# Kernel optimization log

Hardware: AMD Instinct MI355X
Metric: run time of the kernel (lower is better)

The kernel has to match this reference:

```python
import jax, jax.numpy as jnp
import numpy as np

B, L, H, D_IN = 64, 4096, 128, 3

def setup_inputs() -> dict:
    key = jax.random.key(0)
    ks = jax.random.split(key, 9)
    def lin_w(k, fan_in, shape):
        bound = 1.0 / np.sqrt(fan_in)
        return jax.random.uniform(k, shape, jnp.float32, -bound, bound)
    return {
        "x": jax.random.normal(ks[0], (B, L, D_IN), jnp.float32),
        "Wp": lin_w(ks[1], D_IN, (D_IN, H)), "bp": lin_w(ks[2], D_IN, (H,)),
        "Wz": lin_w(ks[3], H, (H, H)),      "bz": lin_w(ks[4], H, (H,)),
        "Wh": lin_w(ks[5], H, (H, H)),      "bh": lin_w(ks[6], H, (H,)),
        "Wg": lin_w(ks[7], H, (H, 1)),      "bg": lin_w(ks[8], H, (1,)),
    }

def reference(x, Wp, bp, Wz, bz, Wh, bh, Wg, bg):
    # Batched projections across all timesteps (B, L, H)
    inp = x @ Wp + bp                      # input_proj
    z = jax.nn.sigmoid(inp @ Wz + bz)      # update gate
    h_tilde = jnp.tanh(inp @ Wh + bh)      # candidate
    # Linear recurrence h_t = a_t * h_{t-1} + b_t, h_{-1} = 0
    a = 1.0 - z
    b = z * h_tilde
    def combine(c1, c2):
        a1, b1 = c1
        a2, b2 = c2
        return (a1 * a2, b1 * a2 + b2)
    _, h = jax.lax.associative_scan(combine, (a, b), axis=1)  # h_t (since h_{-1}=0)
    # Readout uses h BEFORE the update at each step: preds_t = gauss_head(h_{t-1})
    h_prev = jnp.concatenate([jnp.zeros_like(h[:, :1]), h[:, :-1]], axis=1)
    preds = h_prev @ Wg + bg               # (B, L, 1)
    return preds
```

## Files before the change

### kernel.cpp

```cpp
#include <hip/hip_runtime.h>
#include <hip/hip_bf16.h>
#include <stdint.h>

#define B_   64
#define L_   4096
#define H_   128
#define T_   64
#define C_   (L_/T_)
#define BH_  (B_*H_)
#define PADI 136

typedef __attribute__((ext_vector_type(8))) short short8;
typedef __attribute__((ext_vector_type(4))) short short4v;
typedef __attribute__((ext_vector_type(4))) float floatx4;
typedef __attribute__((ext_vector_type(2))) float floatx2;

#define LOG2E 1.44269504088896340736f

__device__ __forceinline__ unsigned short f2bf(float f){
    unsigned int u = __float_as_uint(f);
    u += 0x7FFFu + ((u >> 16) & 1u);
    return (unsigned short)(u >> 16);
}
__device__ __forceinline__ float bf2f(unsigned short s){
    return __uint_as_float(((unsigned int)s) << 16);
}

__global__ void prep_w(const float* __restrict__ Wz, const float* __restrict__ Wh,
                       unsigned short* __restrict__ WzT, unsigned short* __restrict__ WhT){
    int b = blockIdx.x;
    const float* W = (b < 16) ? Wz : Wh;
    unsigned short* WT = (b < 16) ? WzT : WhT;
    int b16 = b & 15, tid = threadIdx.x;
    #pragma unroll
    for (int it = 0; it < 4; ++it){
        int idx = b16*1024 + it*256 + tid;
        int n = idx >> 7, k = idx & 127;
        WT[idx] = f2bf(W[k*H_ + n]);
    }
}

__global__ __launch_bounds__(256, 4)
void carry_kogge(const floatx2* __restrict__ agg2, float* __restrict__ carry_g){
    const int row  = blockIdx.x*4 + (threadIdx.x >> 6);
    const int lane = threadIdx.x & 63;
    floatx2 v = agg2[(size_t)row*C_ + lane];
    #pragma unroll
    for (int d = 1; d < 64; d <<= 1){
        float oA = __shfl_up(v[0], d, 64);
        float oH = __shfl_up(v[1], d, 64);
        if (lane >= d){
            v[1] = fmaf(oH, v[0], v[1]);
            v[0] = oA * v[0];
        }
    }
    float eh = __shfl_up(v[1], 1, 64);
    carry_g[(size_t)row*C_ + lane] = (lane == 0) ? 0.0f : eh;
}


__global__ __launch_bounds__(256, 4)
void gates_agg(const float* __restrict__ x,
               const float* __restrict__ Wp, const float* __restrict__ bp,
               const float* __restrict__ bz, const float* __restrict__ bh,
               const float* __restrict__ Wg,
               const unsigned short* __restrict__ WzT,
               const unsigned short* __restrict__ WhT,
               floatx2* __restrict__ agg2,
               float* __restrict__ sloc, unsigned short* __restrict__ pw_g)
{
    __shared__ __align__(16) unsigned short s_ab[H_*H_];
    __shared__ float s_bz[H_], s_bh[H_], s_wg[H_];
    __shared__ float s_part[256];
    unsigned short* inp_lds = s_ab;

    const int bid = blockIdx.x;
    const int bb  = bid / C_;
    const int cc  = bid % C_;
    const int t0g = cc * T_;
    const int tid = threadIdx.x;
    const int wv = tid >> 6, lane = tid & 63, quad = lane >> 4, l15 = lane & 15;

    if (tid < H_){ s_bz[tid] = bz[tid]; s_bh[tid] = bh[tid]; s_wg[tid] = Wg[tid]; }

    {
        const int h0 = (tid & 15) * 8;
        float w0[8], w1[8], w2[8], b0[8];
        #pragma unroll
        for (int m = 0; m < 8; ++m){
            w0[m] = Wp[h0+m]; w1[m] = Wp[H_+h0+m]; w2[m] = Wp[2*H_+h0+m];
            b0[m] = bp[h0+m];
        }
        #pragma unroll
        for (int it = 0; it < 4; ++it){
            int t = (tid >> 4) + it*16;
            const float* xr = x + ((size_t)bb*L_ + t0g + t)*3;
            float x0 = xr[0], x1 = xr[1], x2 = xr[2];
            short8 pk;
            #pragma unroll
            for (int m = 0; m < 8; ++m){
                float v = b0[m];
                v = fmaf(x0, w0[m], v);
                v = fmaf(x1, w1[m], v);
                v = fmaf(x2, w2[m], v);
                pk[m] = (short)f2bf(v);
            }
            *(short8*)&inp_lds[t*PADI + h0] = pk;
        }
    }
    __syncthreads();

    const int ct0 = wv*2;

    floatx4 accz[4][2], acch[4][2];
    #pragma unroll
    for (int r = 0; r < 4; ++r)
        #pragma unroll
        for (int c = 0; c < 2; ++c){
            accz[r][c] = (floatx4){0.f,0.f,0.f,0.f};
            acch[r][c] = (floatx4){0.f,0.f,0.f,0.f};
        }
    #pragma unroll
    for (int kk = 0; kk < 4; ++kk){
        short8 af[4], bz_[2], bh_[2];
        #pragma unroll
        for (int r = 0; r < 4; ++r)
            af[r] = *(const short8*)&inp_lds[(r*16 + l15)*PADI + kk*32 + quad*8];
        #pragma unroll
        for (int c = 0; c < 2; ++c){
            bz_[c] = *(const short8*)&WzT[((ct0+c)*16 + l15)*H_ + kk*32 + quad*8];
            bh_[c] = *(const short8*)&WhT[((ct0+c)*16 + l15)*H_ + kk*32 + quad*8];
        }
        #pragma unroll
        for (int r = 0; r < 4; ++r)
            #pragma unroll
            for (int c = 0; c < 2; ++c){
                accz[r][c] = __builtin_amdgcn_mfma_f32_16x16x32_bf16(af[r], bz_[c], accz[r][c], 0, 0, 0);
                acch[r][c] = __builtin_amdgcn_mfma_f32_16x16x32_bf16(af[r], bh_[c], acch[r][c], 0, 0, 0);
            }
    }
    __syncthreads();

    #pragma unroll
    for (int r = 0; r < 4; ++r){
        #pragma unroll
        for (int c = 0; c < 2; ++c){
            int col = (ct0+c)*16 + l15;
            float vbz = s_bz[col], vbh = s_bh[col];
            short8 pk;
            #pragma unroll
            for (int e = 0; e < 4; ++e){
                float szb = accz[r][c][e] + vbz;
                float a = __builtin_amdgcn_rcpf(1.0f + __builtin_amdgcn_exp2f(szb * LOG2E));
                float shb = acch[r][c][e] + vbh;
                float ex = __builtin_amdgcn_exp2f(2.0f*LOG2E*shb);
                float th = 1.0f - 2.0f*__builtin_amdgcn_rcpf(ex + 1.0f);
                float bt = (1.0f - a) * th;
                pk[2*e]   = (short)f2bf(a);
                pk[2*e+1] = (short)f2bf(bt);
            }
            int ch = (r*4 + quad) ^ l15;
            *(short8*)&s_ab[col*H_ + ch*8] = pk;
        }
    }
    __syncthreads();

    if (tid < H_){
        float A = 1.0f, h = 0.0f;
        float wgv = s_wg[tid];
        #pragma unroll
        for (int t4 = 0; t4 < 16; ++t4){
            int base = tid*H_ + ((t4 ^ (tid & 15)) << 3);
            short8 pr = *(const short8*)&s_ab[base];
            short8 wb;
            #pragma unroll
            for (int e = 0; e < 4; ++e){
                float aa = bf2f((unsigned short)pr[2*e]);
                float bv = bf2f((unsigned short)pr[2*e+1]);
                wb[2*e]   = (short)f2bf(h * wgv);
                wb[2*e+1] = (short)f2bf(A * wgv);
                A *= aa;
                h = fmaf(aa, h, bv);
            }
            *(short8*)&s_ab[base] = wb;
        }
        agg2[(size_t)(bb*H_ + tid)*C_ + cc] = (floatx2){A, h};
    }
    __syncthreads();

    {
        unsigned short* dst = pw_g + (size_t)bid*(T_*H_);
        #pragma unroll
        for (int i = 0; i < 8; ++i){
            int idx = i*256 + tid;
            int col = idx >> 4, t4 = idx & 15;
            short8 pr = *(const short8*)&s_ab[col*H_ + ((t4 ^ (col & 15)) << 3)];
            short4v pw4;
            pw4[0] = pr[1]; pw4[1] = pr[3]; pw4[2] = pr[5]; pw4[3] = pr[7];
            *(short4v*)&dst[col*T_ + t4*4] = pw4;
        }
    }

    {
        int t = tid & 63, w4 = tid >> 6;
        int t4 = t >> 2, e2 = (t & 3)*2;
        float s = 0.0f;
        #pragma unroll
        for (int j = 0; j < 32; ++j){
            int col = w4*32 + j;
            s += bf2f(s_ab[col*H_ + ((t4 ^ (col & 15)) << 3) + e2]);
        }
        s_part[w4*64 + t] = s;
    }
    __syncthreads();
    if (tid < 64)
        sloc[(size_t)bid*T_ + tid] =
            s_part[tid] + s_part[64+tid] + s_part[128+tid] + s_part[192+tid];
}

__global__ __launch_bounds__(256, 4)
void apply2(const unsigned short* __restrict__ pw_g,
            const float* __restrict__ carry_g,
            const float* __restrict__ sloc, const float* __restrict__ bg,
            float* __restrict__ preds)
{
    __shared__ float s_c[4][H_];
    __shared__ float s_part[4][256];
    const int bid = blockIdx.x;
    const int bb  = bid >> 4;
    const int c4  = bid & 15;
    const int tid = threadIdx.x;
    const int wv = tid >> 6, lane = tid & 63;
    const int cl = lane >> 3, t8 = lane & 7;

    #pragma unroll
    for (int i = 0; i < 2; ++i){
        int idx = tid + i*256;
        int k = idx & 3, h = idx >> 2;
        s_c[k][h] = carry_g[(size_t)(bb*H_ + h)*C_ + c4 + 16*k];
    }
    __syncthreads();

    #pragma unroll
    for (int k = 0; k < 4; ++k){
        const int chunk = c4 + 16*k;
        const unsigned short* src = pw_g + (size_t)(bb*C_ + chunk)*(T_*H_);
        float s8[8];
        #pragma unroll
        for (int e = 0; e < 8; ++e) s8[e] = 0.0f;
        #pragma unroll
        for (int g = 0; g < 4; ++g){
            int col = wv*32 + g*8 + cl;
            short8 pw8 = *(const short8*)&src[col*T_ + t8*8];
            float cv = s_c[k][col];
            #pragma unroll
            for (int e = 0; e < 8; ++e)
                s8[e] = fmaf(cv, bf2f((unsigned short)pw8[e]), s8[e]);
        }
        #pragma unroll
        for (int d = 8; d < 64; d <<= 1)
            #pragma unroll
            for (int e = 0; e < 8; ++e)
                s8[e] += __shfl_xor(s8[e], d, 64);
        if (lane < 8){
            #pragma unroll
            for (int e = 0; e < 8; ++e)
                s_part[k][wv*64 + t8*8 + e] = s8[e];
        }
    }
    __syncthreads();

    {
        int k = tid >> 6, t = tid & 63;
        float s = s_part[k][t] + s_part[k][64+t] + s_part[k][128+t] + s_part[k][192+t];
        int chunk = c4 + 16*k;
        preds[(size_t)bb*L_ + chunk*T_ + t] =
            s + sloc[(size_t)(bb*C_ + chunk)*T_ + t] + bg[0];
    }
}

extern "C" void kernel_launch(void* const* d_in, const int* in_sizes, int n_in,
                              void* d_out, int out_size, void* d_ws, size_t ws_size,
                              hipStream_t stream){
    const float* x  = (const float*)d_in[0];
    const float* Wp = (const float*)d_in[1];
    const float* bp = (const float*)d_in[2];
    const float* Wz = (const float*)d_in[3];
    const float* bz = (const float*)d_in[4];
    const float* Wh = (const float*)d_in[5];
    const float* bh = (const float*)d_in[6];
    const float* Wg = (const float*)d_in[7];
    const float* bg = (const float*)d_in[8];
    float* preds = (float*)d_out;

    uint8_t* w8 = (uint8_t*)d_ws;
    unsigned short* WzT = (unsigned short*)(w8);
    unsigned short* WhT = (unsigned short*)(w8 + 32768);
    floatx2* agg2 = (floatx2*)(w8 + 65536);
    float* sloc   = (float*)(w8 + 65536 + 8u*BH_*C_);
    float* carry  = (float*)(w8 + 65536 + 12u*BH_*C_);
    unsigned short* pw_g = (unsigned short*)(w8 + 65536 + 16u*BH_*C_);

    hipLaunchKernelGGL(prep_w, dim3(32), dim3(256), 0, stream, Wz, Wh, WzT, WhT);
    hipLaunchKernelGGL(gates_agg, dim3(B_*C_), dim3(256), 0, stream,
                       x, Wp, bp, bz, bh, Wg, WzT, WhT, agg2, sloc, pw_g);
    hipLaunchKernelGGL(carry_kogge, dim3(BH_/4), dim3(256), 0, stream, agg2, carry);
    hipLaunchKernelGGL(apply2, dim3(B_*C_/4), dim3(256), 0, stream,
                       pw_g, carry, sloc, bg, preds);
}
```

Baseline: 153.7 us.

## Fuse gates, scan and readout into one sequential per-batch kernel

Replaces the chunked three-kernel pipeline (gates plus local aggregates, cross-chunk Kogge-Stone carry, apply pass) with one kernel per (batch, 32-hidden group). Each 1024-thread block walks 16 time tiles of 256 steps in order, carrying the hidden state in registers. Per tile it computes gates with MFMA, does a two-level in-LDS scan, and writes per-group readout partials, which a small gather kernel sums. This removes the large global pw/agg/carry intermediates and a launch. In exchange only 256 blocks run, the time loop is serial with many barriers per tile, and the projection and GEMM inputs are recomputed for each hidden group.

```diff
diff --git a/kernel.cpp b/kernel.cpp
--- a/kernel.cpp
+++ b/kernel.cpp
@@ -5,9 +5,10 @@
 #define B_   64
 #define L_   4096
 #define H_   128
-#define T_   64
-#define C_   (L_/T_)
-#define BH_  (B_*H_)
+#define HG_  32
+#define NG_  4
+#define TI_  256
+#define NIT_ 16
 #define PADI 136
 
 typedef __attribute__((ext_vector_type(8))) short short8;
@@ -40,243 +41,200 @@
     }
 }
 
-__global__ __launch_bounds__(256, 4)
-void carry_kogge(const floatx2* __restrict__ agg2, float* __restrict__ carry_g){
-    const int row  = blockIdx.x*4 + (threadIdx.x >> 6);
-    const int lane = threadIdx.x & 63;
-    floatx2 v = agg2[(size_t)row*C_ + lane];
-    #pragma unroll
-    for (int d = 1; d < 64; d <<= 1){
-        float oA = __shfl_up(v[0], d, 64);
-        float oH = __shfl_up(v[1], d, 64);
-        if (lane >= d){
-            v[1] = fmaf(oH, v[0], v[1]);
-            v[0] = oA * v[0];
-        }
-    }
-    float eh = __shfl_up(v[1], 1, 64);
-    carry_g[(size_t)row*C_ + lane] = (lane == 0) ? 0.0f : eh;
-}
-
-
-__global__ __launch_bounds__(256, 4)
-void gates_agg(const float* __restrict__ x,
+__global__ __launch_bounds__(1024, 4)
+void fused_rnn(const float* __restrict__ x,
                const float* __restrict__ Wp, const float* __restrict__ bp,
                const float* __restrict__ bz, const float* __restrict__ bh,
                const float* __restrict__ Wg,
                const unsigned short* __restrict__ WzT,
                const unsigned short* __restrict__ WhT,
-               floatx2* __restrict__ agg2,
-               float* __restrict__ sloc, unsigned short* __restrict__ pw_g)
+               float* __restrict__ partials)
 {
-    __shared__ __align__(16) unsigned short s_ab[H_*H_];
-    __shared__ float s_bz[H_], s_bh[H_], s_wg[H_];
-    __shared__ float s_part[256];
-    unsigned short* inp_lds = s_ab;
+    __shared__ __align__(16) unsigned short s_inp[TI_*PADI];
+    __shared__ __align__(16) unsigned int  s_ab[TI_*HG_];
+    __shared__ __align__(16) floatx2 s_agg[32*32];
+    __shared__ float s_hh[32*32];
 
     const int bid = blockIdx.x;
-    const int bb  = bid / C_;
-    const int cc  = bid % C_;
-    const int t0g = cc * T_;
+    const int bb  = bid >> 2;
+    const int g   = bid & 3;
     const int tid = threadIdx.x;
     const int wv = tid >> 6, lane = tid & 63, quad = lane >> 4, l15 = lane & 15;
 
-    if (tid < H_){ s_bz[tid] = bz[tid]; s_bh[tid] = bh[tid]; s_wg[tid] = Wg[tid]; }
+    const int G   = wv >> 3;
+    const int tt0 = wv & 7;
+    const int sh  = tid & 31;
+    const int ss  = tid >> 5;
+    const int rh  = tid >> 5;
+    const int rs  = tid & 31;
+    const int cg  = tid & 31;
+    const int tg  = tid >> 5;
+    const int rt  = tid >> 2;
+    const int rp  = tid & 3;
+
+    const unsigned short* WT = G ? WhT : WzT;
+    short8 bfr[2][4];
+    #pragma unroll
+    for (int ct = 0; ct < 2; ++ct)
+        #pragma unroll
+        for (int kk = 0; kk < 4; ++kk)
+            bfr[ct][kk] = *(const short8*)&WT[(g*HG_ + ct*16 + l15)*H_ + kk*32 + quad*8];
+    float biasv[2];
+    #pragma unroll
+    for (int ct = 0; ct < 2; ++ct)
+        biasv[ct] = (G ? bh : bz)[g*HG_ + ct*16 + l15];
+    const float wgv = Wg[g*HG_ + sh];
+    float w0[4], w1[4], w2[4], bc[4];
+    #pragma unroll
+    for (int m = 0; m < 4; ++m){
+        w0[m] = Wp[cg*4+m]; w1[m] = Wp[H_+cg*4+m]; w2[m] = Wp[2*H_+cg*4+m];
+        bc[m] = bp[cg*4+m];
+    }
+    float h_run = 0.0f;
+
+    for (int it = 0; it < NIT_; ++it){
+        if (it > 0){
+            float s = 0.0f;
+            #pragma unroll
+            for (int i = 0; i < 8; ++i){
+                int col = rp*8 + i;
+                s += ((const float*)s_ab)[rt*HG_ + (col ^ (rt & 31))];
+            }
+            s += __shfl_xor(s, 1);
+            s += __shfl_xor(s, 2);
+            if (rp == 0)
+                partials[(((size_t)(g*B_ + bb)) << 12) + (it-1)*TI_ + rt] = s;
+        }
+        {
+            const float* xr0 = x + ((size_t)bb*L_ + it*TI_ + tg*8)*3;
+            #pragma unroll
+            for (int j = 0; j < 8; ++j){
+                int t = tg*8 + j;
+                float x0 = xr0[j*3], x1 = xr0[j*3+1], x2 = xr0[j*3+2];
+                short4v pk;
+                #pragma unroll
+                for (int m = 0; m < 4; ++m){
+                    float v = bc[m];
+                    v = fmaf(x0, w0[m], v);
+                    v = fmaf(x1, w1[m], v);
+                    v = fmaf(x2, w2[m], v);
+                    pk[m] = (short)f2bf(v);
+                }
+                *(short4v*)&s_inp[t*PADI + cg*4] = pk;
+            }
+        }
+        __syncthreads();
+
+        #pragma unroll
+        for (int tl = 0; tl < 2; ++tl){
+            int tile = tt0 + tl*8;
+            floatx4 acc0 = (floatx4){0.f,0.f,0.f,0.f};
+            floatx4 acc1 = (floatx4){0.f,0.f,0.f,0.f};
+            #pragma unroll
+            for (int kk = 0; kk < 4; ++kk){
+                short8 af = *(const short8*)&s_inp[(tile*16 + l15)*PADI + kk*32 + quad*8];
+                acc0 = __builtin_amdgcn_mfma_f32_16x16x32_bf16(af, bfr[0][kk], acc0, 0, 0, 0);
+                acc1 = __builtin_amdgcn_mfma_f32_16x16x32_bf16(af, bfr[1][kk], acc1, 0, 0, 0);
+            }
+            #pragma unroll
+            for (int ct = 0; ct < 2; ++ct){
+                floatx4 acc = ct ? acc1 : acc0;
+                int hl = ct*16 + l15;
+                #pragma unroll
+                for (int e = 0; e < 4; ++e){
+                    int t = tile*16 + quad*4 + e;
+                    float v = acc[e] + biasv[ct];
+                    float r;
+                    if (G == 0){
+                        r = __builtin_amdgcn_rcpf(1.0f + __builtin_amdgcn_exp2f(v * LOG2E));
+                    } else {
+                        float ex = __builtin_amdgcn_exp2f(2.0f*LOG2E*v);
+                        r = 1.0f - 2.0f*__builtin_amdgcn_rcpf(ex + 1.0f);
+                    }
+                    ((unsigned short*)s_ab)[(t*HG_ + (hl ^ (t & 31)))*2 + G] = f2bf(r);
+                }
+            }
+        }
+        __syncthreads();
+
+        float aj[8], bj[8];
+        {
+            float A = 1.0f, Q = 0.0f;
+            #pragma unroll
+            for (int j = 0; j < 8; ++j){
+                int t = ss*8 + j;
+                unsigned int u = s_ab[t*HG_ + (sh ^ (t & 31))];
+                float a  = bf2f((unsigned short)(u & 0xffffu));
+                float th = bf2f((unsigned short)(u >> 16));
+                float b  = fmaf(-a, th, th);
+                aj[j] = a; bj[j] = b;
+                Q = fmaf(a, Q, b);
+                A *= a;
+            }
+            s_agg[ss*32 + (sh ^ ss)] = (floatx2){A, Q};
+        }
+        __syncthreads();
+
+        {
+            floatx2 v = s_agg[rs*32 + (rh ^ rs)];
+            float P = v[0], Hq = v[1];
+            #pragma unroll
+            for (int d = 1; d < 32; d <<= 1){
+                float pP = __shfl_up(P, d, 32);
+                float pH = __shfl_up(Hq, d, 32);
+                if (rs >= d){
+                    Hq = fmaf(P, pH, Hq);
+                    P  = P * pP;
+                }
+            }
+            float eP = __shfl_up(P, 1, 32);
+            float eH = __shfl_up(Hq, 1, 32);
+            if (rs == 0){ eP = 1.0f; eH = 0.0f; }
+            float tP = __shfl(P, 31, 32);
+            float tH = __shfl(Hq, 31, 32);
+            s_hh[rs*32 + (rh ^ rs)] = fmaf(eP, h_run, eH);
+            h_run = fmaf(tP, h_run, tH);
+        }
+        __syncthreads();
+
+        {
+            float hh = s_hh[ss*32 + (sh ^ ss)];
+            #pragma unroll
+            for (int j = 0; j < 8; ++j){
+                int t = ss*8 + j;
+                ((float*)s_ab)[t*HG_ + (sh ^ (t & 31))] = wgv * hh;
+                hh = fmaf(aj[j], hh, bj[j]);
+            }
+        }
+        __syncthreads();
+    }
 
     {
-        const int h0 = (tid & 15) * 8;
-        float w0[8], w1[8], w2[8], b0[8];
-        #pragma unroll
-        for (int m = 0; m < 8; ++m){
-            w0[m] = Wp[h0+m]; w1[m] = Wp[H_+h0+m]; w2[m] = Wp[2*H_+h0+m];
-            b0[m] = bp[h0+m];
-        }
-        #pragma unroll
-        for (int it = 0; it < 4; ++it){
-            int t = (tid >> 4) + it*16;
-            const float* xr = x + ((size_t)bb*L_ + t0g + t)*3;
-            float x0 = xr[0], x1 = xr[1], x2 = xr[2];
-            short8 pk;
-            #pragma unroll
-            for (int m = 0; m < 8; ++m){
-                float v = b0[m];
-                v = fmaf(x0, w0[m], v);
-                v = fmaf(x1, w1[m], v);
-                v = fmaf(x2, w2[m], v);
-                pk[m] = (short)f2bf(v);
-            }
-            *(short8*)&inp_lds[t*PADI + h0] = pk;
-        }
-    }
-    __syncthreads();
-
-    const int ct0 = wv*2;
-
-    floatx4 accz[4][2], acch[4][2];
-    #pragma unroll
-    for (int r = 0; r < 4; ++r)
-        #pragma unroll
-        for (int c = 0; c < 2; ++c){
-            accz[r][c] = (floatx4){0.f,0.f,0.f,0.f};
-            acch[r][c] = (floatx4){0.f,0.f,0.f,0.f};
-        }
-    #pragma unroll
-    for (int kk = 0; kk < 4; ++kk){
-        short8 af[4], bz_[2], bh_[2];
-        #pragma unroll
-        for (int r = 0; r < 4; ++r)
-            af[r] = *(const short8*)&inp_lds[(r*16 + l15)*PADI + kk*32 + quad*8];
-        #pragma unroll
-        for (int c = 0; c < 2; ++c){
-            bz_[c] = *(const short8*)&WzT[((ct0+c)*16 + l15)*H_ + kk*32 + quad*8];
-            bh_[c] = *(const short8*)&WhT[((ct0+c)*16 + l15)*H_ + kk*32 + quad*8];
-        }
-        #pragma unroll
-        for (int r = 0; r < 4; ++r)
-            #pragma unroll
-            for (int c = 0; c < 2; ++c){
-                accz[r][c] = __builtin_amdgcn_mfma_f32_16x16x32_bf16(af[r], bz_[c], accz[r][c], 0, 0, 0);
-                acch[r][c] = __builtin_amdgcn_mfma_f32_16x16x32_bf16(af[r], bh_[c], acch[r][c], 0, 0, 0);
-            }
-    }
-    __syncthreads();
-
-    #pragma unroll
-    for (int r = 0; r < 4; ++r){
-        #pragma unroll
-        for (int c = 0; c < 2; ++c){
-            int col = (ct0+c)*16 + l15;
-            float vbz = s_bz[col], vbh = s_bh[col];
-            short8 pk;
-            #pragma unroll
-            for (int e = 0; e < 4; ++e){
-                float szb = accz[r][c][e] + vbz;
-                float a = __builtin_amdgcn_rcpf(1.0f + __builtin_amdgcn_exp2f(szb * LOG2E));
-                float shb = acch[r][c][e] + vbh;
-                float ex = __builtin_amdgcn_exp2f(2.0f*LOG2E*shb);
-                float th = 1.0f - 2.0f*__builtin_amdgcn_rcpf(ex + 1.0f);
-                float bt = (1.0f - a) * th;
-                pk[2*e]   = (short)f2bf(a);
-                pk[2*e+1] = (short)f2bf(bt);
-            }
-            int ch = (r*4 + quad) ^ l15;
-            *(short8*)&s_ab[col*H_ + ch*8] = pk;
-        }
-    }
-    __syncthreads();
-
-    if (tid < H_){
-        float A = 1.0f, h = 0.0f;
-        float wgv = s_wg[tid];
-        #pragma unroll
-        for (int t4 = 0; t4 < 16; ++t4){
-            int base = tid*H_ + ((t4 ^ (tid & 15)) << 3);
-            short8 pr = *(const short8*)&s_ab[base];
-            short8 wb;
-            #pragma unroll
-            for (int e = 0; e < 4; ++e){
-                float aa = bf2f((unsigned short)pr[2*e]);
-                float bv = bf2f((unsigned short)pr[2*e+1]);
-                wb[2*e]   = (short)f2bf(h * wgv);
-                wb[2*e+1] = (short)f2bf(A * wgv);
-                A *= aa;
-                h = fmaf(aa, h, bv);
-            }
-            *(short8*)&s_ab[base] = wb;
-        }
-        agg2[(size_t)(bb*H_ + tid)*C_ + cc] = (floatx2){A, h};
-    }
-    __syncthreads();
-
-    {
-        unsigned short* dst = pw_g + (size_t)bid*(T_*H_);
+        float s = 0.0f;
         #pragma unroll
         for (int i = 0; i < 8; ++i){
-            int idx = i*256 + tid;
-            int col = idx >> 4, t4 = idx & 15;
-            short8 pr = *(const short8*)&s_ab[col*H_ + ((t4 ^ (col & 15)) << 3)];
-            short4v pw4;
-            pw4[0] = pr[1]; pw4[1] = pr[3]; pw4[2] = pr[5]; pw4[3] = pr[7];
-            *(short4v*)&dst[col*T_ + t4*4] = pw4;
-        }
-    }
-
-    {
-        int t = tid & 63, w4 = tid >> 6;
-        int t4 = t >> 2, e2 = (t & 3)*2;
-        float s = 0.0f;
-        #pragma unroll
-        for (int j = 0; j < 32; ++j){
-            int col = w4*32 + j;
-            s += bf2f(s_ab[col*H_ + ((t4 ^ (col & 15)) << 3) + e2]);
-        }
-        s_part[w4*64 + t] = s;
-    }
-    __syncthreads();
-    if (tid < 64)
-        sloc[(size_t)bid*T_ + tid] =
-            s_part[tid] + s_part[64+tid] + s_part[128+tid] + s_part[192+tid];
-}
-
-__global__ __launch_bounds__(256, 4)
-void apply2(const unsigned short* __restrict__ pw_g,
-            const float* __restrict__ carry_g,
-            const float* __restrict__ sloc, const float* __restrict__ bg,
+            int col = rp*8 + i;
+            s += ((const float*)s_ab)[rt*HG_ + (col ^ (rt & 31))];
+        }
+        s += __shfl_xor(s, 1);
+        s += __shfl_xor(s, 2);
+        if (rp == 0)
+            partials[(((size_t)(g*B_ + bb)) << 12) + (NIT_-1)*TI_ + rt] = s;
+    }
+}
+
+__global__ __launch_bounds__(1024)
+void gather(const float* __restrict__ partials, const float* __restrict__ bg,
             float* __restrict__ preds)
 {
-    __shared__ float s_c[4][H_];
-    __shared__ float s_part[4][256];
-    const int bid = blockIdx.x;
-    const int bb  = bid >> 4;
-    const int c4  = bid & 15;
-    const int tid = threadIdx.x;
-    const int wv = tid >> 6, lane = tid & 63;
-    const int cl = lane >> 3, t8 = lane & 7;
-
-    #pragma unroll
-    for (int i = 0; i < 2; ++i){
-        int idx = tid + i*256;
-        int k = idx & 3, h = idx >> 2;
-        s_c[k][h] = carry_g[(size_t)(bb*H_ + h)*C_ + c4 + 16*k];
-    }
-    __syncthreads();
-
-    #pragma unroll
-    for (int k = 0; k < 4; ++k){
-        const int chunk = c4 + 16*k;
-        const unsigned short* src = pw_g + (size_t)(bb*C_ + chunk)*(T_*H_);
-        float s8[8];
-        #pragma unroll
-        for (int e = 0; e < 8; ++e) s8[e] = 0.0f;
-        #pragma unroll
-        for (int g = 0; g < 4; ++g){
-            int col = wv*32 + g*8 + cl;
-            short8 pw8 = *(const short8*)&src[col*T_ + t8*8];
-            float cv = s_c[k][col];
-            #pragma unroll
-            for (int e = 0; e < 8; ++e)
-                s8[e] = fmaf(cv, bf2f((unsigned short)pw8[e]), s8[e]);
-        }
-        #pragma unroll
-        for (int d = 8; d < 64; d <<= 1)
-            #pragma unroll
-            for (int e = 0; e < 8; ++e)
-                s8[e] += __shfl_xor(s8[e], d, 64);
-        if (lane < 8){
-            #pragma unroll
-            for (int e = 0; e < 8; ++e)
-                s_part[k][wv*64 + t8*8 + e] = s8[e];
-        }
-    }
-    __syncthreads();
-
-    {
-        int k = tid >> 6, t = tid & 63;
-        float s = s_part[k][t] + s_part[k][64+t] + s_part[k][128+t] + s_part[k][192+t];
-        int chunk = c4 + 16*k;
-        preds[(size_t)bb*L_ + chunk*T_ + t] =
-            s + sloc[(size_t)(bb*C_ + chunk)*T_ + t] + bg[0];
-    }
+    size_t idx = (size_t)blockIdx.x*1024 + threadIdx.x;
+    const size_t GSTRIDE = (size_t)B_ * L_;
+    float s = bg[0];
+    s += partials[idx];
+    s += partials[GSTRIDE + idx];
+    s += partials[2*GSTRIDE + idx];
+    s += partials[3*GSTRIDE + idx];
+    preds[idx] = s;
 }
 
 extern "C" void kernel_launch(void* const* d_in, const int* in_sizes, int n_in,
@@ -296,15 +254,11 @@
     uint8_t* w8 = (uint8_t*)d_ws;
     unsigned short* WzT = (unsigned short*)(w8);
     unsigned short* WhT = (unsigned short*)(w8 + 32768);
-    floatx2* agg2 = (floatx2*)(w8 + 65536);
-    float* sloc   = (float*)(w8 + 65536 + 8u*BH_*C_);
-    float* carry  = (float*)(w8 + 65536 + 12u*BH_*C_);
-    unsigned short* pw_g = (unsigned short*)(w8 + 65536 + 16u*BH_*C_);
+    float* partials = (float*)(w8 + 65536);
 
     hipLaunchKernelGGL(prep_w, dim3(32), dim3(256), 0, stream, Wz, Wh, WzT, WhT);
-    hipLaunchKernelGGL(gates_agg, dim3(B_*C_), dim3(256), 0, stream,
-                       x, Wp, bp, bz, bh, Wg, WzT, WhT, agg2, sloc, pw_g);
-    hipLaunchKernelGGL(carry_kogge, dim3(BH_/4), dim3(256), 0, stream, agg2, carry);
-    hipLaunchKernelGGL(apply2, dim3(B_*C_/4), dim3(256), 0, stream,
-                       pw_g, carry, sloc, bg, preds);
-}
+    hipLaunchKernelGGL(fused_rnn, dim3(B_*NG_), dim3(1024), 0, stream,
+                       x, Wp, bp, bz, bh, Wg, WzT, WhT, partials);
+    hipLaunchKernelGGL(gather, dim3(B_*L_/1024), dim3(1024), 0, stream,
+                       partials, bg, preds);
+}
```

Measured after the change: 153.0 us. No clear change (-0.5%).
